# Optimization experiments

Hardware: AMD Instinct MI355X
Metric: run time of the kernel (lower is better)

## Reference

```python
import jax, jax.numpy as jnp
import numpy as np

N_H, N_O, D = 5000, 15000, 1024
E_HH, E_OO, E_HO = 20000, 40000, 40000


def setup_inputs() -> dict:
    key = jax.random.key(0)
    ks = jax.random.split(key, 20)
    N = N_H + N_O
    w = lambda k, shp: jax.random.normal(k, shp, dtype=jnp.float32) * 0.02
    inp = {
        'n_f': jax.random.normal(ks[0], (N, D), dtype=jnp.float32),
        'src_hh': jax.random.randint(ks[1], (E_HH,), 0, N_H),
        'dst_hh': jax.random.randint(ks[2], (E_HH,), 0, N_H),
        'src_oo': jax.random.randint(ks[3], (E_OO,), 0, N_O) + N_H,
        'dst_oo': jax.random.randint(ks[4], (E_OO,), 0, N_O) + N_H,
        'src_ho': jax.random.randint(ks[5], (E_HO,), 0, N_H),
        'dst_ho': jax.random.randint(ks[6], (E_HO,), 0, N_O) + N_H,
        'W_hh': w(ks[7], (2 * D, D)), 'b_hh': jnp.zeros((D,), jnp.float32),
        'W_oo': w(ks[8], (2 * D, D)), 'b_oo': jnp.zeros((D,), jnp.float32),
        'W_ho': w(ks[9], (2 * D, D)), 'b_ho': jnp.zeros((D,), jnp.float32),
        'W_att': w(ks[10], (D, 1)), 'b_att': jnp.zeros((1,), jnp.float32),
        'W_hn': w(ks[11], (2 * D, D)), 'b_hn': jnp.zeros((D,), jnp.float32),
        'W_on': w(ks[12], (2 * D, D)), 'b_on': jnp.zeros((D,), jnp.float32),
    }
    return inp


def reference(n_f, src_hh, dst_hh, src_oo, dst_oo, src_ho, dst_ho,
              W_hh, b_hh, W_oo, b_oo, W_ho, b_ho, W_att, b_att,
              W_hn, b_hn, W_on, b_on):
    N = n_f.shape[0]

    def edge_mlp(src, dst, W, b):
        # gather -> concat -> Linear -> ReLU  (H_H/O_O/H_O EdgeApplyModule)
        feat = jnp.concatenate([n_f[src], n_f[dst]], axis=1)  # [E, 2D]
        return jax.nn.relu(feat @ W + b)                       # [E, D]

    e_f = jnp.concatenate([
        edge_mlp(src_hh, dst_hh, W_hh, b_hh),
        edge_mlp(src_oo, dst_oo, W_oo, b_oo),
        edge_mlp(src_ho, dst_ho, W_ho, b_ho),
    ], axis=0)                                                 # [E, D]
    src = jnp.concatenate([src_hh, src_oo, src_ho])
    dst = jnp.concatenate([dst_hh, dst_oo, dst_ho])

    # E_AttentionModule: per-edge scalar attention logit
    a = (e_f @ W_att + b_att)[:, 0]                            # [E]

    # update_all: per-destination softmax over incoming edges (mailbox softmax)
    seg_max = jax.ops.segment_max(a, dst, num_segments=N)
    seg_max = jnp.where(jnp.isfinite(seg_max), seg_max, 0.0)
    ex = jnp.exp(a - seg_max[dst])
    denom = jax.ops.segment_sum(ex, dst, num_segments=N)
    alpha = ex / jnp.where(denom[dst] == 0, 1.0, denom[dst])   # [E]
    z = jax.ops.segment_sum(alpha[:, None] * n_f[src], dst, num_segments=N)  # [N, D]

    # Node apply: concat(n_f, z_f) -> Linear -> ReLU, separate h/o MLPs
    new_h = jax.nn.relu(jnp.concatenate([n_f[:N_H], z[:N_H]], axis=1) @ W_hn + b_hn)
    new_o = jax.nn.relu(jnp.concatenate([n_f[N_H:], z[N_H:]], axis=1) @ W_on + b_on)
    return jnp.concatenate([new_h, new_o], axis=0)             # [N, D] new_n_f
```

## Files before the change

### kernel.cpp

```cpp
#include <hip/hip_runtime.h>

#define N_H   5000
#define N_O   15000
#define N_TOT 20000
#define DD    1024
#define E_HH  20000
#define E_OO  40000
#define E_HO  40000
#define E_TOT 100000

typedef unsigned short u16;
typedef unsigned int u32;
typedef __attribute__((ext_vector_type(8))) short short8;
typedef __attribute__((ext_vector_type(4))) float f32x4;
typedef const __attribute__((address_space(1))) u32 gas_u32;
typedef __attribute__((address_space(3))) u32 las_u32;

__device__ __forceinline__ float bf2f(u16 u) {
    union { unsigned int i; float f; } v; v.i = ((unsigned int)u) << 16; return v.f;
}
__device__ __forceinline__ u16 f2bf(float f) {
    union { float f; unsigned int i; } v; v.f = f;
    unsigned int u = v.i;
    return (u16)((u + 0x7FFFu + ((u >> 16) & 1u)) >> 16);
}

#define CAST_NB 10000
__global__ void cast_cat(const float* __restrict__ in, u16* __restrict__ out,
                         const int* __restrict__ shh, const int* __restrict__ dhh,
                         const int* __restrict__ soo, const int* __restrict__ doo,
                         const int* __restrict__ sho, const int* __restrict__ dho,
                         int* __restrict__ src_all, int* __restrict__ dst_all,
                         int* __restrict__ deg) {
    int b = blockIdx.x;
    if (b < CAST_NB) {
        size_t i = ((size_t)b * 256 + threadIdx.x) * 8;
        float4 a = *(const float4*)(in + i);
        float4 c = *(const float4*)(in + i + 4);
        u16 o[8] = {f2bf(a.x), f2bf(a.y), f2bf(a.z), f2bf(a.w),
                    f2bf(c.x), f2bf(c.y), f2bf(c.z), f2bf(c.w)};
        *(uint4*)(out + i) = *(const uint4*)o;
        return;
    }
    int e = (b - CAST_NB) * 256 + threadIdx.x;
    if (e >= E_TOT) return;
    int s, d;
    if (e < E_HH)              { s = shh[e];               d = dhh[e]; }
    else if (e < E_HH + E_OO)  { s = soo[e - E_HH];        d = doo[e - E_HH]; }
    else                       { s = sho[e - E_HH - E_OO]; d = dho[e - E_HH - E_OO]; }
    src_all[e] = s; dst_all[e] = d;
    atomicAdd(&deg[d], 1);
}

struct TW  { const float* W; u16* dT; u16* dB; int ld; };
struct TW5 { TW t[5]; };
__global__ void transpose_all(TW5 p) {
    __shared__ float tile[32][33];
    int z = blockIdx.z;
    TW tw = p.t[z >> 1];
    int half = z & 1;
    int bk = blockIdx.x, bn = blockIdx.y;
    int tx = threadIdx.x & 31, ty = threadIdx.x >> 5;
#pragma unroll
    for (int yy = 0; yy < 4; yy++) {
        int k = half * 1024 + bk * 32 + ty + yy * 8;
        int n = bn * 32 + tx;
        tile[ty + yy * 8][tx] = tw.W[(size_t)k * 1024 + n];
    }
    __syncthreads();
    u16* dst = half ? tw.dB : tw.dT;
#pragma unroll
    for (int yy = 0; yy < 4; yy++) {
        int n = bn * 32 + ty + yy * 8;
        int k = bk * 32 + tx;
        dst[(size_t)n * tw.ld + k] = f2bf(tile[tx][ty + yy * 8]);
    }
}

#define PROJ_NBM_H 40
#define PROJ_NBM_O 118
#define PROJ_NBN   24
__launch_bounds__(256)
__global__ void gemm_proj(const u16* __restrict__ Ah, const u16* __restrict__ Ao,
                          const u16* __restrict__ Bth, const u16* __restrict__ Bto,
                          u16* __restrict__ Ch, u16* __restrict__ Co) {
    __shared__ u16 smem[2][128][64];
    int bid = blockIdx.x;
    const u16* A; const u16* Bt; u16* C; int M;
    if (bid < PROJ_NBM_H * PROJ_NBN) { A = Ah; Bt = Bth; C = Ch; M = N_H; }
    else { bid -= PROJ_NBM_H * PROJ_NBN; A = Ao; Bt = Bto; C = Co; M = N_O; }
    int bm = bid / PROJ_NBN, bn = bid % PROJ_NBN;
    int t = threadIdx.x;
    int wave = t >> 6, lane = t & 63;
    int wr = wave >> 1, wc = wave & 1;
    int lm = lane & 15, q = lane >> 4;
    f32x4 acc[4][4] = {};
    int srow = lane >> 3;
    int scol = ((lane & 7) ^ srow) * 8;

    for (int k0 = 0; k0 < 1024; k0 += 64) {
#pragma unroll
        for (int it = 0; it < 4; it++) {
            int chunk = wave * 4 + it;
            int row = chunk * 8 + srow;
            int gr = bm * 128 + row; if (gr >= M) gr = M - 1;
            __builtin_amdgcn_global_load_lds((gas_u32*)(A + (size_t)gr * 1024 + k0 + scol),
                                             (las_u32*)&smem[0][chunk * 8][0], 16, 0, 0);
            __builtin_amdgcn_global_load_lds((gas_u32*)(Bt + (size_t)(bn * 128 + row) * 1024 + k0 + scol),
                                             (las_u32*)&smem[1][chunk * 8][0], 16, 0, 0);
        }
        __syncthreads();
#pragma unroll
        for (int ks = 0; ks < 64; ks += 32) {
            short8 af[4], bfr[4];
            int pc = (((ks >> 3) + q) ^ (lm & 7)) * 8;
#pragma unroll
            for (int i = 0; i < 4; i++)
                af[i] = *(const short8*)&smem[0][wr * 64 + i * 16 + lm][pc];
#pragma unroll
            for (int j = 0; j < 4; j++)
                bfr[j] = *(const short8*)&smem[1][wc * 64 + j * 16 + lm][pc];
#pragma unroll
            for (int i = 0; i < 4; i++)
#pragma unroll
                for (int j = 0; j < 4; j++)
                    acc[i][j] = __builtin_amdgcn_mfma_f32_16x16x32_bf16(af[i], bfr[j], acc[i][j], 0, 0, 0);
        }
        __syncthreads();
    }
    u16* sc = &smem[0][0][0];
#pragma unroll
    for (int i = 0; i < 4; i++)
#pragma unroll
        for (int j = 0; j < 4; j++)
#pragma unroll
            for (int r = 0; r < 4; r++)
                sc[(wr * 64 + i * 16 + q * 4 + r) * 128 + (wc * 64 + j * 16 + lm)] =
                    f2bf(acc[i][j][r]);
    __syncthreads();
#pragma unroll
    for (int it = 0; it < 8; it++) {
        int flat = it * 256 + t;
        int r = flat >> 4, cs = (flat & 15) * 8;
        int grow = bm * 128 + r;
        if (grow < M)
            *(uint4*)&C[(size_t)grow * 3072 + bn * 128 + cs] = *(const uint4*)&sc[r * 128 + cs];
    }
}

#define NODE_NBM_H 40
#define NODE_NBM_O 118
#define NODE_NBN   8
__launch_bounds__(256)
__global__ void gemm_node(const u16* __restrict__ nf_h, const u16* __restrict__ nf_o,
                          const u16* __restrict__ z_h, const u16* __restrict__ z_o,
                          const u16* __restrict__ Bthn, const u16* __restrict__ Bton,
                          const float* __restrict__ b_hn, const float* __restrict__ b_on,
                          float* __restrict__ out_h, float* __restrict__ out_o) {
    __shared__ u16 lA[128][64];
    __shared__ u16 lB[128][64];
    int bid = (blockIdx.x & 7) * ((NODE_NBM_H + NODE_NBM_O) * NODE_NBN / 8)
            + (blockIdx.x >> 3);
    const u16 *A0, *A1, *Bt; const float* bias; float* C; int M;
    if (bid < NODE_NBM_H * NODE_NBN) {
        A0 = nf_h; A1 = z_h; Bt = Bthn; bias = b_hn; C = out_h; M = N_H;
    } else {
        bid -= NODE_NBM_H * NODE_NBN;
        A0 = nf_o; A1 = z_o; Bt = Bton; bias = b_on; C = out_o; M = N_O;
    }
    int bm = bid / NODE_NBN, bn = bid % NODE_NBN;
    int t = threadIdx.x;
    int wave = t >> 6, lane = t & 63;
    int wr = wave >> 1, wc = wave & 1;
    int lm = lane & 15, q = lane >> 4;
    f32x4 acc[4][4] = {};
    int srow = lane >> 3;
    int scol = ((lane & 7) ^ srow) * 8;

    for (int half = 0; half < 2; half++) {
        const u16* Asrc = half ? A1 : A0;
        const u16* Bth = Bt + half * 1024;
        for (int k0 = 0; k0 < 1024; k0 += 64) {
#pragma unroll
            for (int it = 0; it < 4; it++) {
                int chunk = wave * 4 + it;
                int row = chunk * 8 + srow;
                int gr = bm * 128 + row; if (gr >= M) gr = M - 1;
                __builtin_amdgcn_global_load_lds((gas_u32*)(Asrc + (size_t)gr * 1024 + k0 + scol),
                                                 (las_u32*)&lA[chunk * 8][0], 16, 0, 0);
                __builtin_amdgcn_global_load_lds((gas_u32*)(Bth + (size_t)(bn * 128 + row) * 2048 + k0 + scol),
                                                 (las_u32*)&lB[chunk * 8][0], 16, 0, 0);
            }
            __syncthreads();
#pragma unroll
            for (int ks = 0; ks < 64; ks += 32) {
                short8 af[4], bfr[4];
                int pc = (((ks >> 3) + q) ^ (lm & 7)) * 8;
#pragma unroll
                for (int i = 0; i < 4; i++)
                    af[i] = *(const short8*)&lA[wr * 64 + i * 16 + lm][pc];
#pragma unroll
                for (int j = 0; j < 4; j++)
                    bfr[j] = *(const short8*)&lB[wc * 64 + j * 16 + lm][pc];
#pragma unroll
                for (int i = 0; i < 4; i++)
#pragma unroll
                    for (int j = 0; j < 4; j++)
                        acc[i][j] = __builtin_amdgcn_mfma_f32_16x16x32_bf16(af[i], bfr[j], acc[i][j], 0, 0, 0);
            }
            __syncthreads();
        }
    }
#pragma unroll
    for (int j = 0; j < 4; j++) {
        int col = bn * 128 + wc * 64 + j * 16 + lm;
        float bv = bias[col];
#pragma unroll
        for (int i = 0; i < 4; i++) {
            int row0 = bm * 128 + wr * 64 + i * 16 + q * 4;
#pragma unroll
            for (int r = 0; r < 4; r++) {
                int row = row0 + r;
                if (row < M)
                    C[(size_t)row * 1024 + col] = fmaxf(acc[i][j][r] + bv, 0.0f);
            }
        }
    }
}

__global__ void edge_att(const u16* __restrict__ proj_h, const u16* __restrict__ proj_o,
                         const float* __restrict__ b_hh, const float* __restrict__ b_oo,
                         const float* __restrict__ b_ho,
                         const float* __restrict__ W_att, const float* __restrict__ b_att,
                         const int* __restrict__ src_all, const int* __restrict__ dst_all,
                         float* __restrict__ a_out) {
    int wave = threadIdx.x >> 6, lane = threadIdx.x & 63;
    int e0 = blockIdx.x * 32 + wave * 8;
    const float* bsel = (e0 < E_HH) ? b_hh : (e0 < E_HH + E_OO ? b_oo : b_ho);
    float ww[16], bb[16];
#pragma unroll
    for (int i = 0; i < 16; i++) { ww[i] = W_att[lane * 16 + i]; bb[i] = bsel[lane * 16 + i]; }
    float batt = b_att[0];
#pragma unroll
    for (int k = 0; k < 8; k++) {
        int e = e0 + k;
        int s = src_all[e], d = dst_all[e];
        const u16 *u, *v;
        if (e < E_HH) {
            u = proj_h + (size_t)s * 3072;
            v = proj_h + (size_t)d * 3072 + 1024;
        } else if (e < E_HH + E_OO) {
            u = proj_o + (size_t)(s - N_H) * 3072;
            v = proj_o + (size_t)(d - N_H) * 3072 + 1024;
        } else {
            u = proj_h + (size_t)s * 3072 + 2048;
            v = proj_o + (size_t)(d - N_H) * 3072 + 2048;
        }
        int off = lane * 16;
        uint4 u0 = *(const uint4*)(u + off), u1 = *(const uint4*)(u + off + 8);
        uint4 v0 = *(const uint4*)(v + off), v1 = *(const uint4*)(v + off + 8);
        const u16* pu0 = (const u16*)&u0; const u16* pu1 = (const u16*)&u1;
        const u16* pv0 = (const u16*)&v0; const u16* pv1 = (const u16*)&v1;
        float acc = 0.f;
#pragma unroll
        for (int i = 0; i < 8; i++) {
            float tv = bf2f(pu0[i]) + bf2f(pv0[i]) + bb[i];
            acc += fmaxf(tv, 0.f) * ww[i];
        }
#pragma unroll
        for (int i = 0; i < 8; i++) {
            float tv = bf2f(pu1[i]) + bf2f(pv1[i]) + bb[8 + i];
            acc += fmaxf(tv, 0.f) * ww[8 + i];
        }
#pragma unroll
        for (int o = 32; o > 0; o >>= 1) acc += __shfl_down(acc, o);
        if (lane == 0) a_out[e] = acc + batt;
    }
}

__global__ void scan_deg(const int* __restrict__ deg, int* __restrict__ indptr) {
    __shared__ int sums[1024];
    int t = threadIdx.x;
    const int CH = 20;
    int beg = t * CH, end = beg + CH;
    if (end > N_TOT) end = N_TOT;
    if (beg > N_TOT) beg = N_TOT;
    int s = 0;
    for (int i = beg; i < end; i++) s += deg[i];
    sums[t] = s;
    __syncthreads();
    for (int off = 1; off < 1024; off <<= 1) {
        int v = sums[t];
        int add = (t >= off) ? sums[t - off] : 0;
        __syncthreads();
        sums[t] = v + add;
        __syncthreads();
    }
    int run = (t == 0) ? 0 : sums[t - 1];
    for (int i = beg; i < end; i++) { indptr[i] = run; run += deg[i]; }
    if (t == 1023) indptr[N_TOT] = sums[1023];
}

__global__ void fill_csr(const int* __restrict__ dst_all, const int* __restrict__ indptr,
                         int* __restrict__ cursor, int* __restrict__ edge_ids) {
    int e = blockIdx.x * 256 + threadIdx.x;
    if (e < E_TOT) {
        int d = dst_all[e];
        int pos = atomicAdd(&cursor[d], 1);
        edge_ids[indptr[d] + pos] = e;
    }
}

#define MAXDEG 1024
__global__ void soft_z(const float* __restrict__ a, const int* __restrict__ indptr,
                       const int* __restrict__ edge_ids, const int* __restrict__ src_all,
                       const u16* __restrict__ nf, u16* __restrict__ z) {
    __shared__ float s_a[MAXDEG];
    __shared__ int   s_src[MAXDEG];
    __shared__ float s_inv;
    int node = blockIdx.x;
    int t = threadIdx.x;
    int beg = indptr[node], end = indptr[node + 1];
    int deg = end - beg; if (deg > MAXDEG) deg = MAXDEG;
    if (t < 64) {
        float m = -1e30f;
        for (int i = t; i < deg; i += 64) {
            int eid = edge_ids[beg + i];
            float av = a[eid];
            s_a[i] = av;
            s_src[i] = src_all[eid];
            if (av > m) m = av;
        }
        for (int o = 32; o > 0; o >>= 1) m = fmaxf(m, __shfl_down(m, o));
        m = __shfl(m, 0);
        float ssum = 0.f;
        for (int i = t; i < deg; i += 64) {
            float ex = __expf(s_a[i] - m);
            s_a[i] = ex;
            ssum += ex;
        }
        for (int o = 32; o > 0; o >>= 1) ssum += __shfl_down(ssum, o);
        if (t == 0) s_inv = (ssum > 0.f) ? 1.0f / ssum : 0.f;
    }
    __syncthreads();
    float a0 = 0.f, a1 = 0.f, a2 = 0.f, a3 = 0.f;
    int base = t * 4;
    float inv = s_inv;
    for (int i = 0; i < deg; i++) {
        float al = s_a[i] * inv;
        const u16* row = nf + (size_t)s_src[i] * DD + base;
        uint2 p = *(const uint2*)row;
        const u16* pp = (const u16*)&p;
        a0 += al * bf2f(pp[0]); a1 += al * bf2f(pp[1]);
        a2 += al * bf2f(pp[2]); a3 += al * bf2f(pp[3]);
    }
    uint2 ov;
    u16* po = (u16*)&ov;
    po[0] = f2bf(a0); po[1] = f2bf(a1); po[2] = f2bf(a2); po[3] = f2bf(a3);
    *(uint2*)(z + (size_t)node * DD + base) = ov;
}

extern "C" void kernel_launch(void* const* d_in, const int* in_sizes, int n_in,
                              void* d_out, int out_size, void* d_ws, size_t ws_size,
                              hipStream_t stream) {
    const float* nf   = (const float*)d_in[0];
    const int* shh    = (const int*)d_in[1];
    const int* dhh    = (const int*)d_in[2];
    const int* soo    = (const int*)d_in[3];
    const int* doo    = (const int*)d_in[4];
    const int* sho    = (const int*)d_in[5];
    const int* dho    = (const int*)d_in[6];
    const float* W_hh = (const float*)d_in[7];
    const float* b_hh = (const float*)d_in[8];
    const float* W_oo = (const float*)d_in[9];
    const float* b_oo = (const float*)d_in[10];
    const float* W_ho = (const float*)d_in[11];
    const float* b_ho = (const float*)d_in[12];
    const float* W_att= (const float*)d_in[13];
    const float* b_att= (const float*)d_in[14];
    const float* W_hn = (const float*)d_in[15];
    const float* b_hn = (const float*)d_in[16];
    const float* W_on = (const float*)d_in[17];
    const float* b_on = (const float*)d_in[18];
    float* out = (float*)d_out;

    char* ws = (char*)d_ws;
    size_t off = 0;
    auto alloc = [&](size_t bytes) -> char* {
        char* p = ws + off;
        off += (bytes + 255) & ~(size_t)255;
        return p;
    };
    u16* nf_bf = (u16*)alloc((size_t)N_TOT * DD * 2);
    u16* Bt_h  = (u16*)alloc((size_t)3072 * 1024 * 2);
    u16* Bt_o  = (u16*)alloc((size_t)3072 * 1024 * 2);
    u16* Bt_hn = (u16*)alloc((size_t)1024 * 2048 * 2);
    u16* Bt_on = (u16*)alloc((size_t)1024 * 2048 * 2);
    u16* proj_h = (u16*)alloc((size_t)N_H * 3072 * 2);
    u16* proj_o = (u16*)alloc((size_t)N_O * 3072 * 2);
    u16* z_bf   = proj_h;
    float* a_log  = (float*)alloc(E_TOT * 4);
    int* src_all  = (int*)alloc(E_TOT * 4);
    int* dst_all  = (int*)alloc(E_TOT * 4);
    int* deg      = (int*)alloc(2 * N_TOT * 4);
    int* cursor   = deg + N_TOT;
    int* indptr   = (int*)alloc((N_TOT + 1) * 4);
    int* edge_ids = (int*)alloc(E_TOT * 4);
    (void)ws_size; (void)in_sizes; (void)n_in; (void)out_size;

    hipMemsetAsync(deg, 0, 2 * N_TOT * 4, stream);
    cast_cat<<<CAST_NB + (E_TOT + 255) / 256, 256, 0, stream>>>(
        nf, nf_bf, shh, dhh, soo, doo, sho, dho, src_all, dst_all, deg);

    TW5 tws;
    tws.t[0] = {W_hh, Bt_h,                       Bt_h + (size_t)1024 * 1024, 1024};
    tws.t[1] = {W_oo, Bt_o,                       Bt_o + (size_t)1024 * 1024, 1024};
    tws.t[2] = {W_ho, Bt_h + (size_t)2048 * 1024, Bt_o + (size_t)2048 * 1024, 1024};
    tws.t[3] = {W_hn, Bt_hn,                      Bt_hn + 1024,               2048};
    tws.t[4] = {W_on, Bt_on,                      Bt_on + 1024,               2048};
    transpose_all<<<dim3(32, 32, 10), 256, 0, stream>>>(tws);

    const u16* nf_bf_o = nf_bf + (size_t)N_H * DD;
    gemm_proj<<<(PROJ_NBM_H + PROJ_NBM_O) * PROJ_NBN, 256, 0, stream>>>(
        nf_bf, nf_bf_o, Bt_h, Bt_o, proj_h, proj_o);

    edge_att<<<E_TOT / 32, 256, 0, stream>>>(proj_h, proj_o, b_hh, b_oo, b_ho,
                                             W_att, b_att, src_all, dst_all, a_log);

    scan_deg<<<1, 1024, 0, stream>>>(deg, indptr);
    fill_csr<<<(E_TOT + 255) / 256, 256, 0, stream>>>(dst_all, indptr, cursor, edge_ids);

    soft_z<<<N_TOT, 256, 0, stream>>>(a_log, indptr, edge_ids, src_all, nf_bf, z_bf);

    gemm_node<<<(NODE_NBM_H + NODE_NBM_O) * NODE_NBN, 256, 0, stream>>>(
        nf_bf, nf_bf_o, z_bf, z_bf + (size_t)N_H * DD, Bt_hn, Bt_on,
        b_hn, b_on, out, out + (size_t)N_H * DD);
}
```

Baseline: 609.9 us.

## Fuse edge attention logits into per-destination softmax aggregation kernel

Removes the separate edge_att kernel and computes each edge's attention logit inside the per-node aggregation kernel, walking the destination's CSR edge list with one wave per edge. The destination-side projection row is loaded once per node and reused across all incoming edges, and the a_log round trip through global memory goes away. z now gets its own buffer instead of aliasing proj_h, since proj_h is still being read during aggregation. CSR construction is moved ahead of the projection GEMM. The cost is per-node blocks doing serial wave loops over edges, which may balance poorly across low-degree nodes.

```diff
diff --git a/kernel.cpp b/kernel.cpp
--- a/kernel.cpp
+++ b/kernel.cpp
@@ -228,56 +228,6 @@
     }
 }
 
-__global__ void edge_att(const u16* __restrict__ proj_h, const u16* __restrict__ proj_o,
-                         const float* __restrict__ b_hh, const float* __restrict__ b_oo,
-                         const float* __restrict__ b_ho,
-                         const float* __restrict__ W_att, const float* __restrict__ b_att,
-                         const int* __restrict__ src_all, const int* __restrict__ dst_all,
-                         float* __restrict__ a_out) {
-    int wave = threadIdx.x >> 6, lane = threadIdx.x & 63;
-    int e0 = blockIdx.x * 32 + wave * 8;
-    const float* bsel = (e0 < E_HH) ? b_hh : (e0 < E_HH + E_OO ? b_oo : b_ho);
-    float ww[16], bb[16];
-#pragma unroll
-    for (int i = 0; i < 16; i++) { ww[i] = W_att[lane * 16 + i]; bb[i] = bsel[lane * 16 + i]; }
-    float batt = b_att[0];
-#pragma unroll
-    for (int k = 0; k < 8; k++) {
-        int e = e0 + k;
-        int s = src_all[e], d = dst_all[e];
-        const u16 *u, *v;
-        if (e < E_HH) {
-            u = proj_h + (size_t)s * 3072;
-            v = proj_h + (size_t)d * 3072 + 1024;
-        } else if (e < E_HH + E_OO) {
-            u = proj_o + (size_t)(s - N_H) * 3072;
-            v = proj_o + (size_t)(d - N_H) * 3072 + 1024;
-        } else {
-            u = proj_h + (size_t)s * 3072 + 2048;
-            v = proj_o + (size_t)(d - N_H) * 3072 + 2048;
-        }
-        int off = lane * 16;
-        uint4 u0 = *(const uint4*)(u + off), u1 = *(const uint4*)(u + off + 8);
-        uint4 v0 = *(const uint4*)(v + off), v1 = *(const uint4*)(v + off + 8);
-        const u16* pu0 = (const u16*)&u0; const u16* pu1 = (const u16*)&u1;
-        const u16* pv0 = (const u16*)&v0; const u16* pv1 = (const u16*)&v1;
-        float acc = 0.f;
-#pragma unroll
-        for (int i = 0; i < 8; i++) {
-            float tv = bf2f(pu0[i]) + bf2f(pv0[i]) + bb[i];
-            acc += fmaxf(tv, 0.f) * ww[i];
-        }
-#pragma unroll
-        for (int i = 0; i < 8; i++) {
-            float tv = bf2f(pu1[i]) + bf2f(pv1[i]) + bb[8 + i];
-            acc += fmaxf(tv, 0.f) * ww[8 + i];
-        }
-#pragma unroll
-        for (int o = 32; o > 0; o >>= 1) acc += __shfl_down(acc, o);
-        if (lane == 0) a_out[e] = acc + batt;
-    }
-}
-
 __global__ void scan_deg(const int* __restrict__ deg, int* __restrict__ indptr) {
     __shared__ int sums[1024];
     int t = threadIdx.x;
@@ -312,25 +262,73 @@
 }
 
 #define MAXDEG 1024
-__global__ void soft_z(const float* __restrict__ a, const int* __restrict__ indptr,
-                       const int* __restrict__ edge_ids, const int* __restrict__ src_all,
-                       const u16* __restrict__ nf, u16* __restrict__ z) {
+__launch_bounds__(256)
+__global__ void att_agg(const u16* __restrict__ proj_h, const u16* __restrict__ proj_o,
+                        const float* __restrict__ b_hh, const float* __restrict__ b_oo,
+                        const float* __restrict__ b_ho,
+                        const float* __restrict__ W_att, const float* __restrict__ b_att,
+                        const int* __restrict__ indptr, const int* __restrict__ edge_ids,
+                        const int* __restrict__ src_all,
+                        const u16* __restrict__ nf, u16* __restrict__ z) {
     __shared__ float s_a[MAXDEG];
     __shared__ int   s_src[MAXDEG];
     __shared__ float s_inv;
     int node = blockIdx.x;
-    int t = threadIdx.x;
-    int beg = indptr[node], end = indptr[node + 1];
-    int deg = end - beg; if (deg > MAXDEG) deg = MAXDEG;
+    int t = threadIdx.x, wave = t >> 6, lane = t & 63;
+    int isH = node < N_H;
+    int beg = indptr[node];
+    int deg = indptr[node + 1] - beg;
+    if (deg > MAXDEG) deg = MAXDEG;
+
+    int off = lane * 16;
+    float ww[16], bb0[16], bb1[16];
+    const float* bsel0 = isH ? b_hh : b_oo;
+#pragma unroll
+    for (int i = 0; i < 16; i++) { ww[i] = W_att[off + i]; bb0[i] = bsel0[off + i]; }
+#pragma unroll
+    for (int i = 0; i < 16; i++) bb1[i] = isH ? 0.f : b_ho[off + i];
+    const u16* v0src = isH ? proj_h + (size_t)node * 3072 + 1024
+                           : proj_o + (size_t)(node - N_H) * 3072 + 1024;
+    uint4 va0 = *(const uint4*)(v0src + off), va1 = *(const uint4*)(v0src + off + 8);
+    uint4 vb0 = va0, vb1 = va1;
+    if (!isH) {
+        const u16* v1src = proj_o + (size_t)(node - N_H) * 3072 + 2048;
+        vb0 = *(const uint4*)(v1src + off); vb1 = *(const uint4*)(v1src + off + 8);
+    }
+    float batt = b_att[0];
+
+    for (int i = wave; i < deg; i += 4) {
+        int eid = edge_ids[beg + i];
+        int s = src_all[eid];
+        const u16* u; int typ1;
+        if (eid < E_HH)             { u = proj_h + (size_t)s * 3072;               typ1 = 0; }
+        else if (eid < E_HH + E_OO) { u = proj_o + (size_t)(s - N_H) * 3072;       typ1 = 0; }
+        else                        { u = proj_h + (size_t)s * 3072 + 2048;        typ1 = 1; }
+        uint4 u0 = *(const uint4*)(u + off), u1 = *(const uint4*)(u + off + 8);
+        uint4 v0 = typ1 ? vb0 : va0, v1 = typ1 ? vb1 : va1;
+        const u16* pu0 = (const u16*)&u0; const u16* pu1 = (const u16*)&u1;
+        const u16* pv0 = (const u16*)&v0; const u16* pv1 = (const u16*)&v1;
+        float acc = 0.f;
+#pragma unroll
+        for (int j = 0; j < 8; j++) {
+            float b = typ1 ? bb1[j] : bb0[j];
+            float tv = bf2f(pu0[j]) + bf2f(pv0[j]) + b;
+            acc += fmaxf(tv, 0.f) * ww[j];
+        }
+#pragma unroll
+        for (int j = 0; j < 8; j++) {
+            float b = typ1 ? bb1[8 + j] : bb0[8 + j];
+            float tv = bf2f(pu1[j]) + bf2f(pv1[j]) + b;
+            acc += fmaxf(tv, 0.f) * ww[8 + j];
+        }
+#pragma unroll
+        for (int o = 32; o > 0; o >>= 1) acc += __shfl_down(acc, o);
+        if (lane == 0) { s_a[i] = acc + batt; s_src[i] = s; }
+    }
+    __syncthreads();
     if (t < 64) {
         float m = -1e30f;
-        for (int i = t; i < deg; i += 64) {
-            int eid = edge_ids[beg + i];
-            float av = a[eid];
-            s_a[i] = av;
-            s_src[i] = src_all[eid];
-            if (av > m) m = av;
-        }
+        for (int i = t; i < deg; i += 64) m = fmaxf(m, s_a[i]);
         for (int o = 32; o > 0; o >>= 1) m = fmaxf(m, __shfl_down(m, o));
         m = __shfl(m, 0);
         float ssum = 0.f;
@@ -348,8 +346,7 @@
     float inv = s_inv;
     for (int i = 0; i < deg; i++) {
         float al = s_a[i] * inv;
-        const u16* row = nf + (size_t)s_src[i] * DD + base;
-        uint2 p = *(const uint2*)row;
+        uint2 p = *(const uint2*)(nf + (size_t)s_src[i] * DD + base);
         const u16* pp = (const u16*)&p;
         a0 += al * bf2f(pp[0]); a1 += al * bf2f(pp[1]);
         a2 += al * bf2f(pp[2]); a3 += al * bf2f(pp[3]);
@@ -406,7 +403,9 @@
     int* cursor   = deg + N_TOT;
     int* indptr   = (int*)alloc((N_TOT + 1) * 4);
     int* edge_ids = (int*)alloc(E_TOT * 4);
-    (void)ws_size; (void)in_sizes; (void)n_in; (void)out_size;
+    u16* z_sep    = (u16*)alloc((size_t)N_TOT * DD * 2);
+    z_bf = z_sep;
+    (void)ws_size; (void)in_sizes; (void)n_in; (void)out_size; (void)a_log;
 
     hipMemsetAsync(deg, 0, 2 * N_TOT * 4, stream);
     cast_cat<<<CAST_NB + (E_TOT + 255) / 256, 256, 0, stream>>>(
@@ -420,17 +419,16 @@
     tws.t[4] = {W_on, Bt_on,                      Bt_on + 1024,               2048};
     transpose_all<<<dim3(32, 32, 10), 256, 0, stream>>>(tws);
 
+    scan_deg<<<1, 1024, 0, stream>>>(deg, indptr);
+    fill_csr<<<(E_TOT + 255) / 256, 256, 0, stream>>>(dst_all, indptr, cursor, edge_ids);
+
     const u16* nf_bf_o = nf_bf + (size_t)N_H * DD;
     gemm_proj<<<(PROJ_NBM_H + PROJ_NBM_O) * PROJ_NBN, 256, 0, stream>>>(
         nf_bf, nf_bf_o, Bt_h, Bt_o, proj_h, proj_o);
 
-    edge_att<<<E_TOT / 32, 256, 0, stream>>>(proj_h, proj_o, b_hh, b_oo, b_ho,
-                                             W_att, b_att, src_all, dst_all, a_log);
-
-    scan_deg<<<1, 1024, 0, stream>>>(deg, indptr);
-    fill_csr<<<(E_TOT + 255) / 256, 256, 0, stream>>>(dst_all, indptr, cursor, edge_ids);
-
-    soft_z<<<N_TOT, 256, 0, stream>>>(a_log, indptr, edge_ids, src_all, nf_bf, z_bf);
+    att_agg<<<N_TOT, 256, 0, stream>>>(proj_h, proj_o, b_hh, b_oo, b_ho,
+                                       W_att, b_att, indptr, edge_ids, src_all,
+                                       nf_bf, z_bf);
 
     gemm_node<<<(NODE_NBM_H + NODE_NBM_O) * NODE_NBN, 256, 0, stream>>>(
         nf_bf, nf_bf_o, z_bf, z_bf + (size_t)N_H * DD, Bt_hn, Bt_on,
```

New measurement: 751.1 us. 1.23x slower.
